# Optimization experiments

Hardware: AMD Instinct MI355X
Metric: run time of the kernel (lower is better)

## Reference

```python
import jax, jax.numpy as jnp
import numpy as np

N = 32                      # rotation matrix size (n x n)
INPUT_DIM = 512
HIDDEN = 1024
BATCH = 16384
NUM_ANGLES = N * (N - 1) // 2   # 496

# Givens plane indices in the same order as the original double loop:
# i = 0..n-2, j = i+1..n-1 (row-major upper triangle)
_I_IDX, _J_IDX = np.triu_indices(N, k=1)


def setup_inputs() -> dict:
    key = jax.random.key(0)
    k0, k1, k2 = jax.random.split(key, 3)
    x = jax.random.normal(k0, (BATCH, INPUT_DIM), dtype=jnp.float32)
    # nn.Linear weights: fc (hidden, input_dim), fc2 (num_angles, hidden)
    W1 = jax.random.normal(k1, (HIDDEN, INPUT_DIM), dtype=jnp.float32) / np.sqrt(INPUT_DIM)
    b1 = jnp.zeros((HIDDEN,), dtype=jnp.float32)
    W2 = jax.random.normal(k2, (NUM_ANGLES, HIDDEN), dtype=jnp.float32) / np.sqrt(HIDDEN)
    b2 = jnpups = jnp.zeros((NUM_ANGLES,), dtype=jnp.float32)
    return {"x": x, "W1": W1, "b1": b1, "W2": W2, "b2": b2}


def reference(x, W1, b1, W2, b2):
    """Faithful forward: MLP -> angles -> sequential Givens-rotation product.

    Right-multiplying R by the Givens matrix G(i, j, theta) only mixes
    columns i and j of R, so each loop iteration is a 2-column update
    instead of a full [B, n, n] bmm. Same math as the original.
    """
    B = x.shape[0]
    h = jax.nn.relu(x @ W1.T + b1)                 # [B, HIDDEN]
    angles = jnp.mod(h @ W2.T + b2, 2.0 * jnp.pi)  # [B, NUM_ANGLES]
    c_all = jnp.cos(angles).T                      # [A, B]
    s_all = jnp.sin(angles).T                      # [A, B]

    R0 = jnp.tile(jnp.eye(N, dtype=x.dtype), (B, 1, 1))  # [B, n, n]
    i_idx = jnp.asarray(_I_IDX)
    j_idx = jnp.asarray(_J_IDX)

    def step(R, inp):
        i, j, c, s = inp                # scalars i, j; c, s: [B]
        col_i = R[:, :, i]              # [B, n]
        col_j = R[:, :, j]              # [B, n]
        new_i = col_i * c[:, None] + col_j * s[:, None]
        new_j = -col_i * s[:, None] + col_j * c[:, None]
        R = R.at[:, :, i].set(new_i)
        R = R.at[:, :, j].set(new_j)
        return R, None

    R, _ = jax.lax.scan(step, R0, (i_idx, j_idx, c_all, s_all))
    return R
```

## Files before the change

### kernel.cpp

```cpp
#include <hip/hip_runtime.h>
#include <math.h>
#include <utility>

#define BATCH 16384
#define INPUT_DIM 512
#define HIDDEN 1024
#define NROT 32
#define NANG 496

typedef _Float16 half8 __attribute__((ext_vector_type(8)));
typedef _Float16 half4 __attribute__((ext_vector_type(4)));
typedef float    f32x4 __attribute__((ext_vector_type(4)));

__global__ __launch_bounds__(256) void cvt_f32_f16(
    const float* __restrict__ src, _Float16* __restrict__ dst, int n8)
{
    const int i = blockIdx.x * 256 + threadIdx.x;
    if (i < n8) {
        const float4* s = (const float4*)src + (size_t)i * 2;
        const float4 a = s[0], b = s[1];
        half8 h;
        h[0]=(_Float16)a.x; h[1]=(_Float16)a.y; h[2]=(_Float16)a.z; h[3]=(_Float16)a.w;
        h[4]=(_Float16)b.x; h[5]=(_Float16)b.y; h[6]=(_Float16)b.z; h[7]=(_Float16)b.w;
        *(half8*)(dst + (size_t)i * 8) = h;
    }
}

template<int EPI>
__global__ __launch_bounds__(256) void gemm_nt_f16(
    const _Float16* __restrict__ A, const _Float16* __restrict__ B,
    const float* __restrict__ bias, float* __restrict__ Cf,
    _Float16* __restrict__ Ch, int M, int N, int K, int Nout)
{
    constexpr int BK = 32;
    __shared__ _Float16 sA[2][128 * BK];
    __shared__ _Float16 sB[2][128 * BK];

    const int tid = threadIdx.x;
    const int m0 = blockIdx.y * 128;
    const int n0 = blockIdx.x * 128;

    const int rA  = tid >> 2;
    const int k8  = tid & 3;
    const int swW = ((k8 ^ (rA & 3)) << 3);

    half8 rg[4];

    auto load_tile = [&](int kt) {
        const size_t koff = (size_t)kt * BK + k8 * 8;
        rg[0] = *(const half8*)(A + (size_t)(m0 + rA) * K + koff);
        rg[1] = *(const half8*)(A + (size_t)(m0 + rA + 64) * K + koff);
        half8 z;
        #pragma unroll
        for (int j = 0; j < 8; ++j) z[j] = (_Float16)0.f;
        if (EPI == 0 || (n0 + rA) < N)
            rg[2] = *(const half8*)(B + (size_t)(n0 + rA) * K + koff);
        else rg[2] = z;
        if (EPI == 0 || (n0 + rA + 64) < N)
            rg[3] = *(const half8*)(B + (size_t)(n0 + rA + 64) * K + koff);
        else rg[3] = z;
    };

    auto write_tile = [&](int buf) {
        *(half8*)&sA[buf][ rA       * BK + swW] = rg[0];
        *(half8*)&sA[buf][(rA + 64) * BK + swW] = rg[1];
        *(half8*)&sB[buf][ rA       * BK + swW] = rg[2];
        *(half8*)&sB[buf][(rA + 64) * BK + swW] = rg[3];
    };

    const int lane = tid & 63;
    const int wid  = tid >> 6;
    const int wr = wid >> 1, wc = wid & 1;
    const int fr = lane & 15, fq = lane >> 4;
    const int swR   = ((fq ^ (fr & 3)) << 3);
    const int aBase = (wr * 64 + fr) * BK + swR;
    const int bBase = (wc * 64 + fr) * BK + swR;

    f32x4 acc[4][4];
    #pragma unroll
    for (int i = 0; i < 4; ++i)
        #pragma unroll
        for (int j = 0; j < 4; ++j) acc[i][j] = (f32x4)(0.f);

    const int NT = K / BK;
    load_tile(0);
    write_tile(0);
    int cur = 0;

    for (int kt = 0; kt < NT; ++kt) {
        const bool more = (kt + 1 < NT);
        if (more) load_tile(kt + 1);
        __syncthreads();

        half8 a_[4], b_[4];
        #pragma unroll
        for (int f = 0; f < 4; ++f) {
            a_[f] = *(const half8*)&sA[cur][aBase + f * 16 * BK];
            b_[f] = *(const half8*)&sB[cur][bBase + f * 16 * BK];
        }
        #pragma unroll
        for (int fm = 0; fm < 4; ++fm)
            #pragma unroll
            for (int fn = 0; fn < 4; ++fn)
                acc[fm][fn] = __builtin_amdgcn_mfma_f32_16x16x32_f16(
                    a_[fm], b_[fn], acc[fm][fn], 0, 0, 0);

        if (more) write_tile(cur ^ 1);
        cur ^= 1;
    }

    if (EPI == 0) {
        #pragma unroll
        for (int fn = 0; fn < 4; ++fn) {
            const int col = n0 + wc * 64 + fn * 16 + fr;
            const float bv = bias[col];
            #pragma unroll
            for (int fm = 0; fm < 4; ++fm) {
                const int row0 = m0 + wr * 64 + fm * 16 + fq * 4;
                #pragma unroll
                for (int r = 0; r < 4; ++r)
                    Ch[(size_t)(row0 + r) * Nout + col] =
                        (_Float16)fmaxf(acc[fm][fn][r] + bv, 0.f);
            }
        }
    } else {
        #pragma unroll
        for (int fn = 0; fn < 4; ++fn) {
            const int col = n0 + wc * 64 + fn * 16 + fr;
            if (col < Nout) {
                const float bv = bias[col];
                #pragma unroll
                for (int fm = 0; fm < 4; ++fm) {
                    const int row0 = m0 + wr * 64 + fm * 16 + fq * 4;
                    #pragma unroll
                    for (int r = 0; r < 4; ++r)
                        Cf[(size_t)(row0 + r) * Nout + col] = acc[fm][fn][r] + bv;
                }
            }
        }
    }
}

struct IJTbl { unsigned char i[NANG]; unsigned char j[NANG]; };
constexpr IJTbl make_ij_tbl() {
    IJTbl t{};
    int k = 0;
    for (int i = 0; i < NROT - 1; ++i)
        for (int j = i + 1; j < NROT; ++j) { t.i[k] = (unsigned char)i; t.j[k] = (unsigned char)j; ++k; }
    return t;
}
constexpr IJTbl IJT = make_ij_tbl();

#define EVEN_H 4096
#define ODD_H  8192
#define PCM_H  0
#define RF32   2048

template<int M>
__device__ __forceinline__ void rot_fwd(const f32x4 q, float (&v)[NROT]) {
    {
        constexpr int k = 2 * M;
        constexpr int i = IJT.i[k], j = IJT.j[k];
        const float vi = v[i], vj = v[j];
        v[i] = fmaf(q[0], vi,  q[1] * vj);
        v[j] = fmaf(q[0], vj, -q[1] * vi);
    }
    {
        constexpr int k = 2 * M + 1;
        constexpr int i = IJT.i[k], j = IJT.j[k];
        const float vi = v[i], vj = v[j];
        v[i] = fmaf(q[2], vi,  q[3] * vj);
        v[j] = fmaf(q[2], vj, -q[3] * vi);
    }
}

template<int M>
__device__ __forceinline__ void rot_rev(const f32x4 q, float (&v)[NROT]) {
    {
        constexpr int k = 2 * M + 1;
        constexpr int i = IJT.i[k], j = IJT.j[k];
        const float vi = v[i], vj = v[j];
        v[i] = fmaf(q[2], vi, -q[3] * vj);
        v[j] = fmaf(q[2], vj,  q[3] * vi);
    }
    {
        constexpr int k = 2 * M;
        constexpr int i = IJT.i[k], j = IJT.j[k];
        const float vi = v[i], vj = v[j];
        v[i] = fmaf(q[0], vi, -q[1] * vj);
        v[j] = fmaf(q[0], vj,  q[1] * vi);
    }
}

template<int W, int T>
__device__ __forceinline__ void chain_step(const float* __restrict__ lcs,
                                           float (&v)[NROT]) {
    if constexpr ((W & 1) == 0) {
        constexpr int fi = 62 * W + T;
        const f32x4 q = *(const f32x4*)(lcs + fi * 4);
        rot_fwd<fi>(q, v);
    } else {
        constexpr int fi = 62 * W + (61 - T);
        const f32x4 q = *(const f32x4*)(lcs + fi * 4);
        rot_rev<fi>(q, v);
    }
}

template<int W, size_t... Ts>
__device__ __forceinline__ void chain_runW(const float* __restrict__ lcs,
                                           float (&v)[NROT],
                                           std::index_sequence<Ts...>) {
    (chain_step<W, (int)Ts>(lcs, v), ...);
}

template<int W>
__device__ __forceinline__ void chain_and_store(const float* __restrict__ lcs,
                                                _Float16* __restrict__ lh,
                                                int half, int r) {
    float v[NROT];
    #pragma unroll
    for (int c = 0; c < NROT; ++c) v[c] = (c == r) ? 1.f : 0.f;
    chain_runW<W>(lcs, v, std::make_index_sequence<62>{});

    constexpr int REG = ((W & 1) == 0) ? EVEN_H : ODD_H;
    const int base = REG + (half * 2 + (W >> 1)) * 1024;
    #pragma unroll
    for (int kq = 0; kq < 4; ++kq) {
        half8 hv;
        #pragma unroll
        for (int j = 0; j < 8; ++j) hv[j] = (_Float16)v[kq * 8 + j];
        *(half8*)&lh[base + r * 32 + ((kq ^ (r & 3)) << 3)] = hv;
    }
}

__global__ __launch_bounds__(256) void rotate_kernel(
    const float* __restrict__ theta, float* __restrict__ out)
{
    __shared__ float smem[6144];
    _Float16* lh = (_Float16*)smem;

    const int tid  = threadIdx.x;
    const int wid  = tid >> 6;
    const int lane = tid & 63;
    const int half = (tid >> 5) & 1;
    const int r    = tid & 31;
    const int fr = lane & 15, fq = lane >> 4;
    const size_t b0 = (size_t)blockIdx.x * 2;

    if (tid < 248) {
        const f32x4 th = *(const f32x4*)(theta + b0 * NANG + tid * 4);
        f32x4 p0, p1;
        float s, c;
        __sincosf(th[0], &s, &c); p0[0] = c; p0[1] = s;
        __sincosf(th[1], &s, &c); p0[2] = c; p0[3] = s;
        __sincosf(th[2], &s, &c); p1[0] = c; p1[1] = s;
        __sincosf(th[3], &s, &c); p1[2] = c; p1[3] = s;
        *(f32x4*)&smem[tid * 8]     = p0;
        *(f32x4*)&smem[tid * 8 + 4] = p1;
    }
    __syncthreads();

    const float* lcs = smem + half * 992;
    if      (wid == 0) chain_and_store<0>(lcs, lh, half, r);
    else if (wid == 1) chain_and_store<1>(lcs, lh, half, r);
    else if (wid == 2) chain_and_store<2>(lcs, lh, half, r);
    else               chain_and_store<3>(lcs, lh, half, r);
    __syncthreads();

    {
        const int ba = wid >> 1, pi = wid & 1;
        const int Eb = EVEN_H + (ba * 2 + pi) * 1024;
        const int Ob = ODD_H  + (ba * 2 + pi) * 1024;
        const int Asrc = (pi == 0) ? Ob : Eb;
        const int Bsrc = (pi == 0) ? Eb : Ob;
        const int swz = (fq ^ (fr & 3)) << 3;
        half8 a[2], b[2];
        #pragma unroll
        for (int mi = 0; mi < 2; ++mi) {
            a[mi] = *(const half8*)&lh[Asrc + (mi * 16 + fr) * 32 + swz];
            b[mi] = *(const half8*)&lh[Bsrc + (mi * 16 + fr) * 32 + swz];
        }
        const int Pb = PCM_H + (ba * 2 + pi) * 1024;
        #pragma unroll
        for (int mi = 0; mi < 2; ++mi)
            #pragma unroll
            for (int ni = 0; ni < 2; ++ni) {
                const f32x4 d = __builtin_amdgcn_mfma_f32_16x16x32_f16(
                    a[mi], b[ni], (f32x4)(0.f), 0, 0, 0);
                half4 hv;
                #pragma unroll
                for (int q = 0; q < 4; ++q) hv[q] = (_Float16)d[q];
                const int col  = ni * 16 + fr;
                const int rowb = (mi * 16 + fq * 4) ^ ((col & 3) << 3);
                *(half4*)&lh[Pb + col * 32 + rowb] = hv;
            }
    }
    __syncthreads();

    {
        const int ba = wid >> 1, mi = wid & 1;
        const int Ab = PCM_H + (ba * 2 + 1) * 1024;
        const int Bb = PCM_H + (ba * 2 + 0) * 1024;
        const int swz = (fq ^ (fr & 3)) << 3;
        const half8 a = *(const half8*)&lh[Ab + (mi * 16 + fr) * 32 + swz];
        #pragma unroll
        for (int ni = 0; ni < 2; ++ni) {
            const half8 b = *(const half8*)&lh[Bb + (ni * 16 + fr) * 32 + swz];
            const f32x4 d = __builtin_amdgcn_mfma_f32_16x16x32_f16(
                a, b, (f32x4)(0.f), 0, 0, 0);
            const int row  = ni * 16 + fr;
            const int colq = mi * 4 + fq;
            *(f32x4*)&smem[RF32 + ba * 1024 + row * 32 + ((colq ^ (row & 7)) << 2)] = d;
        }
    }
    __syncthreads();

    #pragma unroll
    for (int s = 0; s < 2; ++s) {
        const int idx = s * 256 + tid;
        const int ba  = idx >> 8;
        const int f4i = idx & 255;
        const int row = f4i >> 3;
        const int cc  = f4i & 7;
        const f32x4 val =
            *(const f32x4*)&smem[RF32 + ba * 1024 + row * 32 + ((cc ^ (row & 7)) << 2)];
        *(f32x4*)(out + (b0 + ba) * 1024 + (size_t)f4i * 4) = val;
    }
}

extern "C" void kernel_launch(void* const* d_in, const int* in_sizes, int n_in,
                              void* d_out, int out_size, void* d_ws, size_t ws_size,
                              hipStream_t stream)
{
    const float* x  = (const float*)d_in[0];
    const float* W1 = (const float*)d_in[1];
    const float* b1 = (const float*)d_in[2];
    const float* W2 = (const float*)d_in[3];
    const float* b2 = (const float*)d_in[4];
    float* out = (float*)d_out;

    _Float16* h16  = (_Float16*)d_out;
    _Float16* x16  = h16  + (size_t)BATCH * HIDDEN;
    _Float16* W116 = x16  + (size_t)BATCH * INPUT_DIM;
    _Float16* W216 = W116 + (size_t)HIDDEN * INPUT_DIM;
    float*    th   = (float*)d_ws;

    cvt_f32_f16<<<dim3((BATCH * INPUT_DIM / 8 + 255) / 256), 256, 0, stream>>>(
        x, x16, BATCH * INPUT_DIM / 8);
    cvt_f32_f16<<<dim3((HIDDEN * INPUT_DIM / 8 + 255) / 256), 256, 0, stream>>>(
        W1, W116, HIDDEN * INPUT_DIM / 8);
    cvt_f32_f16<<<dim3((NANG * HIDDEN / 8 + 255) / 256), 256, 0, stream>>>(
        W2, W216, NANG * HIDDEN / 8);

    gemm_nt_f16<0><<<dim3(HIDDEN / 128, BATCH / 128), 256, 0, stream>>>(
        x16, W116, b1, nullptr, h16, BATCH, HIDDEN, INPUT_DIM, HIDDEN);

    gemm_nt_f16<1><<<dim3((NANG + 127) / 128, BATCH / 128), 256, 0, stream>>>(
        h16, W216, b2, th, nullptr, BATCH, NANG, HIDDEN, NANG);

    rotate_kernel<<<dim3(BATCH / 2), 256, 0, stream>>>(th, out);
}
```

Before: 119.5 us.

## Split Givens chains into eight segments per batch with a three-level MFMA product tree

The rotation kernel now runs 512 threads per block and splits each sample's 496 rotations into eight 31-pair segments instead of four 62-pair segments. Each wave builds one partial factor, and the factors are combined in a tree of MFMA matrix products: four products, then two, then one. This halves the serial per-thread rotation chain. In exchange it adds an extra level of fp16 matrix products with more rounding, uses more shared memory, adds barriers, and leaves some waves idle in the later stages.

Measured after the change: 188.2 us. 1.57x slower.

```diff
diff --git a/kernel.cpp b/kernel.cpp
--- a/kernel.cpp
+++ b/kernel.cpp
@@ -151,10 +151,10 @@
 }
 constexpr IJTbl IJT = make_ij_tbl();
 
-#define EVEN_H 4096
-#define ODD_H  8192
-#define PCM_H  0
-#define RF32   2048
+#define FACT_H 4096
+#define PROD_H 0
+#define QH     8192
+#define RF32   0
 
 template<int M>
 __device__ __forceinline__ void rot_fwd(const f32x4 q, float (&v)[NROT]) {
@@ -196,13 +196,13 @@
 __device__ __forceinline__ void chain_step(const float* __restrict__ lcs,
                                            float (&v)[NROT]) {
     if constexpr ((W & 1) == 0) {
-        constexpr int fi = 62 * W + T;
-        const f32x4 q = *(const f32x4*)(lcs + fi * 4);
-        rot_fwd<fi>(q, v);
+        constexpr int M = 31 * W + T;
+        const f32x4 q = *(const f32x4*)(lcs + M * 4);
+        rot_fwd<M>(q, v);
     } else {
-        constexpr int fi = 62 * W + (61 - T);
-        const f32x4 q = *(const f32x4*)(lcs + fi * 4);
-        rot_rev<fi>(q, v);
+        constexpr int M = 31 * W + (30 - T);
+        const f32x4 q = *(const f32x4*)(lcs + M * 4);
+        rot_rev<M>(q, v);
     }
 }
 
@@ -216,14 +216,13 @@
 template<int W>
 __device__ __forceinline__ void chain_and_store(const float* __restrict__ lcs,
                                                 _Float16* __restrict__ lh,
-                                                int half, int r) {
+                                                int ba, int r) {
     float v[NROT];
     #pragma unroll
     for (int c = 0; c < NROT; ++c) v[c] = (c == r) ? 1.f : 0.f;
-    chain_runW<W>(lcs, v, std::make_index_sequence<62>{});
-
-    constexpr int REG = ((W & 1) == 0) ? EVEN_H : ODD_H;
-    const int base = REG + (half * 2 + (W >> 1)) * 1024;
+    chain_runW<W>(lcs, v, std::make_index_sequence<31>{});
+
+    const int base = FACT_H + (ba * 8 + W) * 1024;
     #pragma unroll
     for (int kq = 0; kq < 4; ++kq) {
         half8 hv;
@@ -233,16 +232,16 @@
     }
 }
 
-__global__ __launch_bounds__(256) void rotate_kernel(
+__global__ __launch_bounds__(512) void rotate_kernel(
     const float* __restrict__ theta, float* __restrict__ out)
 {
-    __shared__ float smem[6144];
+    __shared__ float smem[10240];
     _Float16* lh = (_Float16*)smem;
 
     const int tid  = threadIdx.x;
     const int wid  = tid >> 6;
     const int lane = tid & 63;
-    const int half = (tid >> 5) & 1;
+    const int hw   = (tid >> 5) & 1;
     const int r    = tid & 31;
     const int fr = lane & 15, fq = lane >> 4;
     const size_t b0 = (size_t)blockIdx.x * 2;
@@ -260,19 +259,25 @@
     }
     __syncthreads();
 
-    const float* lcs = smem + half * 992;
-    if      (wid == 0) chain_and_store<0>(lcs, lh, half, r);
-    else if (wid == 1) chain_and_store<1>(lcs, lh, half, r);
-    else if (wid == 2) chain_and_store<2>(lcs, lh, half, r);
-    else               chain_and_store<3>(lcs, lh, half, r);
-    __syncthreads();
-
-    {
-        const int ba = wid >> 1, pi = wid & 1;
-        const int Eb = EVEN_H + (ba * 2 + pi) * 1024;
-        const int Ob = ODD_H  + (ba * 2 + pi) * 1024;
-        const int Asrc = (pi == 0) ? Ob : Eb;
-        const int Bsrc = (pi == 0) ? Eb : Ob;
+    const float* lcs = smem + hw * 992;
+    switch (wid) {
+        case 0: chain_and_store<0>(lcs, lh, hw, r); break;
+        case 1: chain_and_store<1>(lcs, lh, hw, r); break;
+        case 2: chain_and_store<2>(lcs, lh, hw, r); break;
+        case 3: chain_and_store<3>(lcs, lh, hw, r); break;
+        case 4: chain_and_store<4>(lcs, lh, hw, r); break;
+        case 5: chain_and_store<5>(lcs, lh, hw, r); break;
+        case 6: chain_and_store<6>(lcs, lh, hw, r); break;
+        default: chain_and_store<7>(lcs, lh, hw, r); break;
+    }
+    __syncthreads();
+
+    {
+        const int ba = wid >> 2, p = wid & 3;
+        const int Eb = FACT_H + (ba * 8 + 2 * p)     * 1024;
+        const int Ob = FACT_H + (ba * 8 + 2 * p + 1) * 1024;
+        const int Asrc = ((p & 1) == 0) ? Ob : Eb;
+        const int Bsrc = ((p & 1) == 0) ? Eb : Ob;
         const int swz = (fq ^ (fr & 3)) << 3;
         half8 a[2], b[2];
         #pragma unroll
@@ -280,7 +285,8 @@
             a[mi] = *(const half8*)&lh[Asrc + (mi * 16 + fr) * 32 + swz];
             b[mi] = *(const half8*)&lh[Bsrc + (mi * 16 + fr) * 32 + swz];
         }
-        const int Pb = PCM_H + (ba * 2 + pi) * 1024;
+        __syncthreads();
+        const int Pb = PROD_H + (ba * 4 + p) * 1024;
         #pragma unroll
         for (int mi = 0; mi < 2; ++mi)
             #pragma unroll
@@ -297,27 +303,57 @@
     }
     __syncthreads();
 
-    {
-        const int ba = wid >> 1, mi = wid & 1;
-        const int Ab = PCM_H + (ba * 2 + 1) * 1024;
-        const int Bb = PCM_H + (ba * 2 + 0) * 1024;
+    if (wid < 4) {
+        const int ba = wid >> 1, qi = wid & 1;
+        const int Asrc = PROD_H + (ba * 4 + (qi == 0 ? 1 : 2)) * 1024;
+        const int Bsrc = PROD_H + (ba * 4 + (qi == 0 ? 0 : 3)) * 1024;
         const int swz = (fq ^ (fr & 3)) << 3;
-        const half8 a = *(const half8*)&lh[Ab + (mi * 16 + fr) * 32 + swz];
-        #pragma unroll
-        for (int ni = 0; ni < 2; ++ni) {
-            const half8 b = *(const half8*)&lh[Bb + (ni * 16 + fr) * 32 + swz];
-            const f32x4 d = __builtin_amdgcn_mfma_f32_16x16x32_f16(
-                a, b, (f32x4)(0.f), 0, 0, 0);
-            const int row  = ni * 16 + fr;
-            const int colq = mi * 4 + fq;
-            *(f32x4*)&smem[RF32 + ba * 1024 + row * 32 + ((colq ^ (row & 7)) << 2)] = d;
-        }
-    }
-    __syncthreads();
-
-    #pragma unroll
-    for (int s = 0; s < 2; ++s) {
-        const int idx = s * 256 + tid;
+        half8 a[2], b[2];
+        #pragma unroll
+        for (int mi = 0; mi < 2; ++mi) {
+            a[mi] = *(const half8*)&lh[Asrc + (mi * 16 + fr) * 32 + swz];
+            b[mi] = *(const half8*)&lh[Bsrc + (mi * 16 + fr) * 32 + swz];
+        }
+        const int Qb = QH + (ba * 2 + qi) * 1024;
+        #pragma unroll
+        for (int mi = 0; mi < 2; ++mi)
+            #pragma unroll
+            for (int ni = 0; ni < 2; ++ni) {
+                const f32x4 d = __builtin_amdgcn_mfma_f32_16x16x32_f16(
+                    a[mi], b[ni], (f32x4)(0.f), 0, 0, 0);
+                half4 hv;
+                #pragma unroll
+                for (int q = 0; q < 4; ++q) hv[q] = (_Float16)d[q];
+                const int col  = ni * 16 + fr;
+                const int rowb = (mi * 16 + fq * 4) ^ ((col & 3) << 3);
+                *(half4*)&lh[Qb + col * 32 + rowb] = hv;
+            }
+    }
+    __syncthreads();
+
+    if (wid < 2) {
+        const int ba = wid;
+        const int Ab = QH + (ba * 2 + 1) * 1024;
+        const int Bb = QH + (ba * 2 + 0) * 1024;
+        const int swz = (fq ^ (fr & 3)) << 3;
+        #pragma unroll
+        for (int mi = 0; mi < 2; ++mi) {
+            const half8 a = *(const half8*)&lh[Ab + (mi * 16 + fr) * 32 + swz];
+            #pragma unroll
+            for (int ni = 0; ni < 2; ++ni) {
+                const half8 b = *(const half8*)&lh[Bb + (ni * 16 + fr) * 32 + swz];
+                const f32x4 d = __builtin_amdgcn_mfma_f32_16x16x32_f16(
+                    a, b, (f32x4)(0.f), 0, 0, 0);
+                const int row  = ni * 16 + fr;
+                const int colq = mi * 4 + fq;
+                *(f32x4*)&smem[RF32 + ba * 1024 + row * 32 + ((colq ^ (row & 7)) << 2)] = d;
+            }
+        }
+    }
+    __syncthreads();
+
+    {
+        const int idx = tid;
         const int ba  = idx >> 8;
         const int f4i = idx & 255;
         const int row = f4i >> 3;
@@ -358,5 +394,5 @@
     gemm_nt_f16<1><<<dim3((NANG + 127) / 128, BATCH / 128), 256, 0, stream>>>(
         h16, W216, b2, th, nullptr, BATCH, NANG, HIDDEN, NANG);
 
-    rotate_kernel<<<dim3(BATCH / 2), 256, 0, stream>>>(th, out);
-}
+    rotate_kernel<<<dim3(BATCH / 2), 512, 0, stream>>>(th, out);
+}
```

## Use direct global-to-LDS loads in GEMMs, fuse conversions, swizzle block order

Applied to the files above, without the earlier changes.

The three fp32-to-fp16 conversion launches are merged into one kernel, which also zero-pads W2 up to 512 rows so the second GEMM no longer needs bounds checks. The GEMM tile staging now uses global_load_lds to copy straight into LDS instead of going through registers, with one barrier per k-step. Blocks are also remapped into groups of 8 along M to improve L2 reuse. The trade-off is that the zero-padded W2 buffer must fit in the output scratch area, and the single sync per iteration must still be enough to order the asynchronous LDS writes.

Measured after the change: 112.2 us. -6.1%, faster.

```diff
diff --git a/kernel.cpp b/kernel.cpp
--- a/kernel.cpp
+++ b/kernel.cpp
@@ -12,64 +12,78 @@
 typedef _Float16 half4 __attribute__((ext_vector_type(4)));
 typedef float    f32x4 __attribute__((ext_vector_type(4)));
 
-__global__ __launch_bounds__(256) void cvt_f32_f16(
-    const float* __restrict__ src, _Float16* __restrict__ dst, int n8)
+#define NX8  (BATCH * INPUT_DIM / 8)
+#define NW18 (HIDDEN * INPUT_DIM / 8)
+#define NW28 (512 * HIDDEN / 8)
+
+__global__ __launch_bounds__(256) void prep_f16(
+    const float* __restrict__ x, const float* __restrict__ W1,
+    const float* __restrict__ W2, _Float16* __restrict__ x16,
+    _Float16* __restrict__ W116, _Float16* __restrict__ W216)
 {
     const int i = blockIdx.x * 256 + threadIdx.x;
-    if (i < n8) {
-        const float4* s = (const float4*)src + (size_t)i * 2;
+    const float* src; _Float16* dst; int j; bool zero = false;
+    if (i < NX8)              { j = i;               src = x;  dst = x16;  }
+    else if (i < NX8 + NW18)  { j = i - NX8;         src = W1; dst = W116; }
+    else if (i < NX8 + NW18 + NW28) {
+        j = i - NX8 - NW18;   src = W2; dst = W216;
+        zero = (j * 8 >= NANG * HIDDEN);
+    } else return;
+
+    half8 h;
+    if (zero) {
+        #pragma unroll
+        for (int q = 0; q < 8; ++q) h[q] = (_Float16)0.f;
+    } else {
+        const float4* s = (const float4*)src + (size_t)j * 2;
         const float4 a = s[0], b = s[1];
-        half8 h;
         h[0]=(_Float16)a.x; h[1]=(_Float16)a.y; h[2]=(_Float16)a.z; h[3]=(_Float16)a.w;
         h[4]=(_Float16)b.x; h[5]=(_Float16)b.y; h[6]=(_Float16)b.z; h[7]=(_Float16)b.w;
-        *(half8*)(dst + (size_t)i * 8) = h;
-    }
+    }
+    *(half8*)(dst + (size_t)j * 8) = h;
+}
+
+__device__ __forceinline__ void gld16(const void* g, void* l) {
+    __builtin_amdgcn_global_load_lds(
+        (const __attribute__((address_space(1))) void*)g,
+        (__attribute__((address_space(3))) void*)l, 16, 0, 0);
 }
 
 template<int EPI>
 __global__ __launch_bounds__(256) void gemm_nt_f16(
     const _Float16* __restrict__ A, const _Float16* __restrict__ B,
     const float* __restrict__ bias, float* __restrict__ Cf,
-    _Float16* __restrict__ Ch, int M, int N, int K, int Nout)
+    _Float16* __restrict__ Ch, int M, int K, int Nout, int GX)
 {
     constexpr int BK = 32;
     __shared__ _Float16 sA[2][128 * BK];
     __shared__ _Float16 sB[2][128 * BK];
 
-    const int tid = threadIdx.x;
-    const int m0 = blockIdx.y * 128;
-    const int n0 = blockIdx.x * 128;
-
-    const int rA  = tid >> 2;
-    const int k8  = tid & 3;
-    const int swW = ((k8 ^ (rA & 3)) << 3);
-
-    half8 rg[4];
-
-    auto load_tile = [&](int kt) {
-        const size_t koff = (size_t)kt * BK + k8 * 8;
-        rg[0] = *(const half8*)(A + (size_t)(m0 + rA) * K + koff);
-        rg[1] = *(const half8*)(A + (size_t)(m0 + rA + 64) * K + koff);
-        half8 z;
-        #pragma unroll
-        for (int j = 0; j < 8; ++j) z[j] = (_Float16)0.f;
-        if (EPI == 0 || (n0 + rA) < N)
-            rg[2] = *(const half8*)(B + (size_t)(n0 + rA) * K + koff);
-        else rg[2] = z;
-        if (EPI == 0 || (n0 + rA + 64) < N)
-            rg[3] = *(const half8*)(B + (size_t)(n0 + rA + 64) * K + koff);
-        else rg[3] = z;
-    };
-
-    auto write_tile = [&](int buf) {
-        *(half8*)&sA[buf][ rA       * BK + swW] = rg[0];
-        *(half8*)&sA[buf][(rA + 64) * BK + swW] = rg[1];
-        *(half8*)&sB[buf][ rA       * BK + swW] = rg[2];
-        *(half8*)&sB[buf][(rA + 64) * BK + swW] = rg[3];
-    };
-
+    const int g  = blockIdx.x;
+    const int my = (g & 7) + (((g >> 3) / GX) << 3);
+    const int mx = (g >> 3) % GX;
+    const int m0 = my * 128;
+    const int n0 = mx * 128;
+
+    const int tid  = threadIdx.x;
     const int lane = tid & 63;
     const int wid  = tid >> 6;
+
+    const int srow = lane >> 2;
+    const int schk = (lane & 3) ^ (srow & 3);
+    const _Float16* gA0 = A + (size_t)(m0 + wid * 32 + srow) * K + schk * 8;
+    const _Float16* gA1 = gA0 + (size_t)16 * K;
+    const _Float16* gB0 = B + (size_t)(n0 + wid * 32 + srow) * K + schk * 8;
+    const _Float16* gB1 = gB0 + (size_t)16 * K;
+
+    auto stage = [&](int kt, int buf) {
+        const size_t ko = (size_t)kt * BK;
+        gld16(gA0 + ko, &sA[buf][wid * 1024]);
+        gld16(gA1 + ko, &sA[buf][wid * 1024 + 512]);
+        gld16(gB0 + ko, &sB[buf][wid * 1024]);
+        gld16(gB1 + ko, &sB[buf][wid * 1024 + 512]);
+    };
+
     const int wr = wid >> 1, wc = wid & 1;
     const int fr = lane & 15, fq = lane >> 4;
     const int swR   = ((fq ^ (fr & 3)) << 3);
@@ -83,14 +97,12 @@
         for (int j = 0; j < 4; ++j) acc[i][j] = (f32x4)(0.f);
 
     const int NT = K / BK;
-    load_tile(0);
-    write_tile(0);
+    stage(0, 0);
+    __syncthreads();
     int cur = 0;
 
     for (int kt = 0; kt < NT; ++kt) {
-        const bool more = (kt + 1 < NT);
-        if (more) load_tile(kt + 1);
-        __syncthreads();
+        if (kt + 1 < NT) stage(kt + 1, cur ^ 1);
 
         half8 a_[4], b_[4];
         #pragma unroll
@@ -105,7 +117,7 @@
                 acc[fm][fn] = __builtin_amdgcn_mfma_f32_16x16x32_f16(
                     a_[fm], b_[fn], acc[fm][fn], 0, 0, 0);
 
-        if (more) write_tile(cur ^ 1);
+        __syncthreads();
         cur ^= 1;
     }
 
@@ -345,18 +357,14 @@
     _Float16* W216 = W116 + (size_t)HIDDEN * INPUT_DIM;
     float*    th   = (float*)d_ws;
 
-    cvt_f32_f16<<<dim3((BATCH * INPUT_DIM / 8 + 255) / 256), 256, 0, stream>>>(
-        x, x16, BATCH * INPUT_DIM / 8);
-    cvt_f32_f16<<<dim3((HIDDEN * INPUT_DIM / 8 + 255) / 256), 256, 0, stream>>>(
-        W1, W116, HIDDEN * INPUT_DIM / 8);
-    cvt_f32_f16<<<dim3((NANG * HIDDEN / 8 + 255) / 256), 256, 0, stream>>>(
-        W2, W216, NANG * HIDDEN / 8);
-
-    gemm_nt_f16<0><<<dim3(HIDDEN / 128, BATCH / 128), 256, 0, stream>>>(
-        x16, W116, b1, nullptr, h16, BATCH, HIDDEN, INPUT_DIM, HIDDEN);
-
-    gemm_nt_f16<1><<<dim3((NANG + 127) / 128, BATCH / 128), 256, 0, stream>>>(
-        h16, W216, b2, th, nullptr, BATCH, NANG, HIDDEN, NANG);
+    prep_f16<<<dim3((NX8 + NW18 + NW28) / 256), 256, 0, stream>>>(
+        x, W1, W2, x16, W116, W216);
+
+    gemm_nt_f16<0><<<dim3(8 * 128), 256, 0, stream>>>(
+        x16, W116, b1, nullptr, h16, BATCH, INPUT_DIM, HIDDEN, 8);
+
+    gemm_nt_f16<1><<<dim3(4 * 128), 256, 0, stream>>>(
+        h16, W216, b2, th, nullptr, BATCH, HIDDEN, NANG, 4);
 
     rotate_kernel<<<dim3(BATCH / 2), 256, 0, stream>>>(th, out);
 }
```
